# Kernel tuning notes

Hardware: AMD Instinct MI355X
Metric: run time of the kernel (lower is better)

## Reference

```python
import jax, jax.numpy as jnp
import numpy as np

AGENT_RADIUS = 0.5
SAFETY_DIST = 0.1
QP_ITERS = 300


def _qp_solve(p, G, h):
    """Batched QP: min_u 0.5 u^T u + p^T u  s.t.  G u <= h  (Q = I).
    Solved in the dual by projected gradient ascent (differentiable, fixed iters).
    p: [B,2], G: [B,m,2], h: [B,m] -> u: [B,2]
    """
    GGt = jnp.einsum('bmi,bni->bmn', G, G)                 # [B,m,m]
    q = jnp.einsum('bmi,bi->bm', G, p) + h                 # [B,m]
    # Lipschitz upper bound per sample (Frobenius norm of GG^T)
    L = jnp.sqrt(jnp.sum(GGt * GGt, axis=(1, 2))) + 1e-6   # [B]
    alpha = (1.0 / L)[:, None]

    def step(lam, _):
        grad = jnp.einsum('bmn,bn->bm', GGt, lam) + q
        lam = jnp.maximum(lam - alpha * grad, 0.0)
        return lam, None

    lam0 = jnp.zeros_like(h)
    lam, _ = jax.lax.scan(step, lam0, None, length=QP_ITERS)
    u = -p - jnp.einsum('bmi,bm->bi', G, lam)
    return u


def setup_inputs() -> dict:
    key = jax.random.key(0)
    ks = jax.random.split(key, 20)
    B, F, H1, H2 = 8192, 8, 1024, 512

    def w(k, i, o):
        return (jax.random.normal(k, (i, o), jnp.float32) / np.sqrt(i)).astype(jnp.float32)

    obs_xy = jax.random.uniform(ks[17], (8, 2), jnp.float32, -10.0, 10.0)
    obs_r = jax.random.uniform(ks[18], (8, 1), jnp.float32, 0.3, 0.8)
    return {
        'x': jax.random.normal(ks[0], (B, F), jnp.float32),
        'mean': 0.1 * jax.random.normal(ks[1], (F,), jnp.float32),
        'std': jax.random.uniform(ks[2], (F,), jnp.float32, 0.5, 1.5),
        'W1': w(ks[3], F, H1), 'b1': jnp.zeros((H1,), jnp.float32),
        'W21': w(ks[4], H1, H2), 'b21': jnp.zeros((H2,), jnp.float32),
        'W22': w(ks[5], H1, H2), 'b22': jnp.zeros((H2,), jnp.float32),
        'W23': w(ks[6], H1, H2), 'b23': jnp.zeros((H2,), jnp.float32),
        'W31': w(ks[7], H2, 2), 'b31': jnp.zeros((2,), jnp.float32),
        'W32': w(ks[8], H2, 2), 'b32': jnp.zeros((2,), jnp.float32),
        'W33': w(ks[9], H2, 1), 'b33': jnp.zeros((1,), jnp.float32),
        'obstacles': jnp.concatenate([obs_xy, obs_r], axis=1),  # [8,3] (x,y,r)
        'sgn': 1,
    }


def reference(x, mean, std, W1, b1, W21, b21, W22, b22, W23, b23,
              W31, b31, W32, b32, W33, b33, obstacles, sgn):
    B = x.shape[0]
    x0 = x * std + mean                                   # un-normalized state [B,8]

    h1 = jax.nn.relu(x @ W1 + b1)
    x21 = jax.nn.relu(h1 @ W21 + b21)
    x22 = jax.nn.relu(h1 @ W22 + b22)
    x23 = jax.nn.relu(h1 @ W23 + b23)
    x31 = x21 @ W31 + b31                                 # QP linear term p [B,2]
    x32 = 4.0 * jax.nn.sigmoid(x22 @ W32 + b32)           # CBF gains p1,p2 [B,2]
    x33 = 4.0 * jax.nn.sigmoid(x23 @ W33 + b33)           # liveness gain (unused, smg off)

    px, py, theta, v = x0[:, 0], x0[:, 1], x0[:, 2], x0[:, 3]
    st, ct = jnp.sin(theta)[:, None], jnp.cos(theta)[:, None]
    vb = v[:, None]

    # static obstacles broadcast to batch + opponent as last obstacle -> [B, m]
    ox = jnp.concatenate([jnp.broadcast_to(obstacles[:, 0][None], (B, obstacles.shape[0])), x0[:, 4:5]], axis=1)
    oy = jnp.concatenate([jnp.broadcast_to(obstacles[:, 1][None], (B, obstacles.shape[0])), x0[:, 5:6]], axis=1)
    orad = jnp.concatenate([jnp.broadcast_to(obstacles[:, 2][None], (B, obstacles.shape[0])),
                            jnp.full((B, 1), AGENT_RADIUS, x0.dtype)], axis=1)

    R = AGENT_RADIUS + orad + SAFETY_DIST
    dx = px[:, None] - ox                                  # [B,m]
    dy = py[:, None] - oy

    barrier = dx * dx + dy * dy - R * R
    barrier_dot = 2.0 * dx * vb * ct + 2.0 * dy * vb * st
    Lf2b = (2.0 * v * v)[:, None]
    LgLfbu1 = -2.0 * dx * vb * st + 2.0 * dy * vb * ct
    LgLfbu2 = 2.0 * dx * ct + 2.0 * dy * st
    G = jnp.stack([-LgLfbu1, -LgLfbu2], axis=-1)           # [B,m,2]
    p1, p2 = x32[:, 0:1], x32[:, 1:2]
    h = Lf2b + (p1 + p2) * barrier_dot + p1 * p2 * barrier # [B,m]

    u = _qp_solve(x31, G, h)                               # [B,2]
    return u
```

## Files before the change

kernel.cpp:

```cpp
#include <hip/hip_runtime.h>
#include <cstdint>
#include <cstddef>

typedef unsigned short u16;
typedef u16   u16x8  __attribute__((ext_vector_type(8)));
typedef u16   u16x4  __attribute__((ext_vector_type(4)));
typedef __bf16 bf16x8 __attribute__((ext_vector_type(8)));
typedef float f32x4  __attribute__((ext_vector_type(4)));
typedef float f32x2  __attribute__((ext_vector_type(2)));

__device__ __forceinline__ float bf2f(u16 v) {
  unsigned int u = ((unsigned int)v) << 16;
  return __builtin_bit_cast(float, u);
}
__device__ __forceinline__ u16 f2bf(float f) {
  unsigned int x = __builtin_bit_cast(unsigned int, f);
  x += 0x7fffu + ((x >> 16) & 1u);
  return (u16)(x >> 16);
}

__device__ __forceinline__ void gld_lds16(const u16* g, u16* l) {
  __builtin_amdgcn_global_load_lds(
      (const __attribute__((address_space(1))) unsigned int*)g,
      (__attribute__((address_space(3))) unsigned int*)l, 16, 0, 0);
}

__global__ __launch_bounds__(256) void k_tr(const float* __restrict__ W21,
                                            const float* __restrict__ W22,
                                            u16* __restrict__ Wt) {
  __shared__ u16 s[64][65];
  const int b   = blockIdx.x;
  const int mat = b >> 7;
  const int tt  = b & 127;
  const int k0  = (tt >> 3) * 64;
  const int n0  = (tt & 7) * 64;
  const float* W = mat ? W22 : W21;
  const int tx = threadIdx.x & 63;
  const int ty = threadIdx.x >> 6;
#pragma unroll
  for (int i = 0; i < 16; ++i) {
    int r = i * 4 + ty;
    s[r][tx] = f2bf(W[(size_t)(k0 + r) * 512 + n0 + tx]);
  }
  __syncthreads();
  const int nbase = mat * 512 + n0;
#pragma unroll
  for (int i = 0; i < 16; ++i) {
    int r = i * 4 + ty;
    Wt[(size_t)(nbase + r) * 1024 + k0 + tx] = s[tx][r];
  }
}

__global__ __launch_bounds__(256) void k_h1(const float* __restrict__ x,
                                            const float* __restrict__ W1,
                                            const float* __restrict__ b1,
                                            u16* __restrict__ h1) {
  const int row = blockIdx.x;
  const int c4  = threadIdx.x * 4;
  const float* xr = x + (size_t)row * 8;
  f32x4 acc = *(const f32x4*)(b1 + c4);
#pragma unroll
  for (int f = 0; f < 8; ++f) {
    float xv = xr[f];
    f32x4 wv = *(const f32x4*)(W1 + f * 1024 + c4);
#pragma unroll
    for (int e = 0; e < 4; ++e) acc[e] = fmaf(xv, wv[e], acc[e]);
  }
  u16x4 o;
#pragma unroll
  for (int e = 0; e < 4; ++e) o[e] = f2bf(fmaxf(acc[e], 0.f));
  *(u16x4*)(h1 + (size_t)row * 1024 + c4) = o;
}

__global__ __launch_bounds__(256) void k_gemm(const u16* __restrict__ A,
                                              const u16* __restrict__ Bt,
                                              const float* __restrict__ b21,
                                              const float* __restrict__ b22,
                                              u16* __restrict__ X2) {
  constexpr int K = 1024;
  constexpr int BK = 32;
  __shared__ u16 As[128 * BK];
  __shared__ u16 Bs[128 * BK];

  const int t    = threadIdx.x;
  const int row0 = blockIdx.y * 128;
  const int col0 = blockIdx.x * 128;
  const int w    = t >> 6;
  const int lane = t & 63;
  const int wr   = w >> 1, wc = w & 1;
  const int lrow = lane & 15;
  const int lk   = (lane >> 4) * 8;

  const int cA0 = t, cA1 = 256 + t;
  const int cB0 = t, cB1 = 256 + t;
  const u16* gA0 = A  + (size_t)(row0 + (cA0 >> 2)) * K + (cA0 & 3) * 8;
  const u16* gA1 = A  + (size_t)(row0 + (cA1 >> 2)) * K + (cA1 & 3) * 8;
  const u16* gB0 = Bt + (size_t)(col0 + (cB0 >> 2)) * K + (cB0 & 3) * 8;
  const u16* gB1 = Bt + (size_t)(col0 + (cB1 >> 2)) * K + (cB1 & 3) * 8;
  u16* lA0 = As + cA0 * 8;
  u16* lA1 = As + cA1 * 8;
  u16* lB0 = Bs + cB0 * 8;
  u16* lB1 = Bs + cB1 * 8;

  f32x4 acc[4][4];
#pragma unroll
  for (int i = 0; i < 4; ++i)
#pragma unroll
    for (int j = 0; j < 4; ++j) acc[i][j] = f32x4{0.f, 0.f, 0.f, 0.f};

  for (int kt = 0; kt < K / BK; ++kt) {
    gld_lds16(gA0, lA0);
    gld_lds16(gA1, lA1);
    gld_lds16(gB0, lB0);
    gld_lds16(gB1, lB1);
    gA0 += BK; gA1 += BK; gB0 += BK; gB1 += BK;
    __syncthreads();

    bf16x8 af[4], bfr[4];
#pragma unroll
    for (int i = 0; i < 4; ++i)
      af[i] = __builtin_bit_cast(bf16x8,
          *(const u16x8*)(As + (wr * 64 + i * 16 + lrow) * BK + lk));
#pragma unroll
    for (int j = 0; j < 4; ++j)
      bfr[j] = __builtin_bit_cast(bf16x8,
          *(const u16x8*)(Bs + (wc * 64 + j * 16 + lrow) * BK + lk));
#pragma unroll
    for (int i = 0; i < 4; ++i)
#pragma unroll
      for (int j = 0; j < 4; ++j)
        acc[i][j] = __builtin_amdgcn_mfma_f32_16x16x32_bf16(af[i], bfr[j], acc[i][j], 0, 0, 0);
    __syncthreads();
  }

#pragma unroll
  for (int j = 0; j < 4; ++j) {
    int col = col0 + wc * 64 + j * 16 + lrow;
    float bias = (col < 512) ? b21[col] : b22[col - 512];
#pragma unroll
    for (int i = 0; i < 4; ++i) {
      int rbase = row0 + wr * 64 + i * 16 + (lane >> 4) * 4;
#pragma unroll
      for (int rr = 0; rr < 4; ++rr) {
        float v = acc[i][j][rr] + bias;
        X2[(size_t)(rbase + rr) * 1024 + col] = f2bf(fmaxf(v, 0.f));
      }
    }
  }
}

__global__ __launch_bounds__(256) void k_head(const u16* __restrict__ X2,
                                              const float* __restrict__ W31,
                                              const float* __restrict__ W32,
                                              float* __restrict__ head) {
  const int wv   = threadIdx.x >> 6;
  const int lane = threadIdx.x & 63;
  const int r    = blockIdx.x * 4 + wv;
  const u16* row = X2 + (size_t)r * 1024;

  u16x8 v0 = *(const u16x8*)(row + lane * 8);
  u16x8 v1 = *(const u16x8*)(row + 512 + lane * 8);
  const f32x4* w31p = (const f32x4*)(W31 + lane * 16);
  const f32x4* w32p = (const f32x4*)(W32 + lane * 16);

  float a0x = 0.f, a0y = 0.f, a1x = 0.f, a1y = 0.f;
#pragma unroll
  for (int i = 0; i < 4; ++i) {
    f32x4 wa = w31p[i];
    float e0 = bf2f(v0[2 * i]), e1 = bf2f(v0[2 * i + 1]);
    a0x = fmaf(e0, wa[0], a0x); a0y = fmaf(e0, wa[1], a0y);
    a0x = fmaf(e1, wa[2], a0x); a0y = fmaf(e1, wa[3], a0y);
    f32x4 wb = w32p[i];
    float f0 = bf2f(v1[2 * i]), f1 = bf2f(v1[2 * i + 1]);
    a1x = fmaf(f0, wb[0], a1x); a1y = fmaf(f0, wb[1], a1y);
    a1x = fmaf(f1, wb[2], a1x); a1y = fmaf(f1, wb[3], a1y);
  }
#pragma unroll
  for (int m = 32; m >= 1; m >>= 1) {
    a0x += __shfl_xor(a0x, m, 64);
    a0y += __shfl_xor(a0y, m, 64);
    a1x += __shfl_xor(a1x, m, 64);
    a1y += __shfl_xor(a1y, m, 64);
  }
  if (lane == 0)
    *(f32x4*)(head + 4 * (size_t)r) = f32x4{a0x, a0y, a1x, a1y};
}

__global__ __launch_bounds__(64) void k_qp(const float* __restrict__ x,
                                           const float* __restrict__ mean_,
                                           const float* __restrict__ std_,
                                           const float* __restrict__ head,
                                           const float* __restrict__ b31,
                                           const float* __restrict__ b32,
                                           const float* __restrict__ obstacles,
                                           float* __restrict__ out) {
  const int r = blockIdx.x * 64 + threadIdx.x;
  f32x4 hd = *(const f32x4*)(head + 4 * (size_t)r);
  float p0  = hd[0] + b31[0];
  float p1v = hd[1] + b31[1];
  float pp1 = 4.f / (1.f + expf(-(hd[2] + b32[0])));
  float pp2 = 4.f / (1.f + expf(-(hd[3] + b32[1])));

  const f32x4* xp = (const f32x4*)(x + (size_t)r * 8);
  f32x4 xa = xp[0], xb = xp[1];
  float px = xa[0] * std_[0] + mean_[0];
  float py = xa[1] * std_[1] + mean_[1];
  float th = xa[2] * std_[2] + mean_[2];
  float v  = xa[3] * std_[3] + mean_[3];
  float ax = xb[0] * std_[4] + mean_[4];
  float ay = xb[1] * std_[5] + mean_[5];
  float st = sinf(th), ct = cosf(th);
  float Lf2b = 2.f * v * v;

  float G0[9], G1[9], q[9];
  float s00 = 0.f, s01 = 0.f, s11 = 0.f;
#pragma unroll
  for (int m = 0; m < 9; ++m) {
    float ox, oy, orad;
    if (m < 8) {
      ox = obstacles[m * 3]; oy = obstacles[m * 3 + 1]; orad = obstacles[m * 3 + 2];
    } else { ox = ax; oy = ay; orad = 0.5f; }
    float R  = 0.6f + orad;
    float dx = px - ox, dy = py - oy;
    float bar  = dx * dx + dy * dy - R * R;
    float dct  = dx * ct + dy * st;
    float bdot = 2.f * v * dct;
    float g0 = 2.f * v * (dx * st - dy * ct);
    float g1 = -2.f * dct;
    float h  = Lf2b + (pp1 + pp2) * bdot + pp1 * pp2 * bar;
    G0[m] = g0; G1[m] = g1;
    q[m] = g0 * p0 + g1 * p1v + h;
    s00 += g0 * g0; s01 += g0 * g1; s11 += g1 * g1;
  }
  float L = sqrtf(s00 * s00 + 2.f * s01 * s01 + s11 * s11) + 1e-6f;
  float alpha = 1.f / L;

  float lam[9];
#pragma unroll
  for (int m = 0; m < 9; ++m) lam[m] = 0.f;
  for (int it = 0; it < 300; ++it) {
    float pr0[9], pr1[9];
#pragma unroll
    for (int m = 0; m < 9; ++m) { pr0[m] = G0[m] * lam[m]; pr1[m] = G1[m] * lam[m]; }
    float t0 = (((pr0[0] + pr0[1]) + (pr0[2] + pr0[3])) +
                ((pr0[4] + pr0[5]) + (pr0[6] + pr0[7]))) + pr0[8];
    float t1 = (((pr1[0] + pr1[1]) + (pr1[2] + pr1[3])) +
                ((pr1[4] + pr1[5]) + (pr1[6] + pr1[7]))) + pr1[8];
#pragma unroll
    for (int m = 0; m < 9; ++m) {
      float g = fmaf(G0[m], t0, fmaf(G1[m], t1, q[m]));
      lam[m] = fmaxf(fmaf(-alpha, g, lam[m]), 0.f);
    }
  }
  float u0 = -p0, u1 = -p1v;
#pragma unroll
  for (int m = 0; m < 9; ++m) { u0 = fmaf(-G0[m], lam[m], u0); u1 = fmaf(-G1[m], lam[m], u1); }
  *(f32x2*)(out + 2 * (size_t)r) = f32x2{u0, u1};
}

extern "C" void kernel_launch(void* const* d_in, const int* in_sizes, int n_in,
                              void* d_out, int out_size, void* d_ws, size_t ws_size,
                              hipStream_t stream) {
  const float* x    = (const float*)d_in[0];
  const float* mean_= (const float*)d_in[1];
  const float* std_ = (const float*)d_in[2];
  const float* W1   = (const float*)d_in[3];
  const float* b1   = (const float*)d_in[4];
  const float* W21  = (const float*)d_in[5];
  const float* b21  = (const float*)d_in[6];
  const float* W22  = (const float*)d_in[7];
  const float* b22  = (const float*)d_in[8];
  const float* W31  = (const float*)d_in[11];
  const float* b31  = (const float*)d_in[12];
  const float* W32  = (const float*)d_in[13];
  const float* b32  = (const float*)d_in[14];
  const float* obst = (const float*)d_in[17];
  float* out = (float*)d_out;

  char* ws = (char*)d_ws;
  u16*   Wt   = (u16*)ws;
  u16*   h1   = (u16*)(ws + (size_t)(1 << 21));
  u16*   X2   = (u16*)(ws + (size_t)(1 << 21) + (size_t)(1 << 24));
  float* head = (float*)(ws + (size_t)(1 << 21) + 2 * (size_t)(1 << 24));

  k_tr  <<<256, 256, 0, stream>>>(W21, W22, Wt);
  k_h1  <<<8192, 256, 0, stream>>>(x, W1, b1, h1);
  k_gemm<<<dim3(8, 64), 256, 0, stream>>>(h1, Wt, b21, b22, X2);
  k_head<<<2048, 256, 0, stream>>>(X2, W31, W32, head);
  k_qp  <<<128, 64, 0, stream>>>(x, mean_, std_, head, b31, b32, obst, out);
}
```

Measured before the change: 172.5 us.

## Double-buffer GEMM LDS tiles with register-staged prefetch two tiles ahead

Replaces the direct global-to-LDS loads in the bf16 MFMA GEMM with ordinary vector loads into registers, staged two K-tiles ahead, and a double-buffered LDS. This removes one barrier per iteration and lets global memory latency overlap with the MFMA work on the current tile. In exchange it uses more registers and twice the LDS, which may lower occupancy, and every element now takes an extra register-to-LDS store.

```diff
diff --git a/kernel.cpp b/kernel.cpp
--- a/kernel.cpp
+++ b/kernel.cpp
@@ -17,12 +17,6 @@
   unsigned int x = __builtin_bit_cast(unsigned int, f);
   x += 0x7fffu + ((x >> 16) & 1u);
   return (u16)(x >> 16);
-}
-
-__device__ __forceinline__ void gld_lds16(const u16* g, u16* l) {
-  __builtin_amdgcn_global_load_lds(
-      (const __attribute__((address_space(1))) unsigned int*)g,
-      (__attribute__((address_space(3))) unsigned int*)l, 16, 0, 0);
 }
 
 __global__ __launch_bounds__(256) void k_tr(const float* __restrict__ W21,
@@ -77,10 +71,11 @@
                                               const float* __restrict__ b21,
                                               const float* __restrict__ b22,
                                               u16* __restrict__ X2) {
-  constexpr int K = 1024;
+  constexpr int K  = 1024;
   constexpr int BK = 32;
-  __shared__ u16 As[128 * BK];
-  __shared__ u16 Bs[128 * BK];
+  constexpr int NT = K / BK;
+  __shared__ u16 As[2][128 * BK];
+  __shared__ u16 Bs[2][128 * BK];
 
   const int t    = threadIdx.x;
   const int row0 = blockIdx.y * 128;
@@ -91,16 +86,12 @@
   const int lrow = lane & 15;
   const int lk   = (lane >> 4) * 8;
 
-  const int cA0 = t, cA1 = 256 + t;
-  const int cB0 = t, cB1 = 256 + t;
-  const u16* gA0 = A  + (size_t)(row0 + (cA0 >> 2)) * K + (cA0 & 3) * 8;
-  const u16* gA1 = A  + (size_t)(row0 + (cA1 >> 2)) * K + (cA1 & 3) * 8;
-  const u16* gB0 = Bt + (size_t)(col0 + (cB0 >> 2)) * K + (cB0 & 3) * 8;
-  const u16* gB1 = Bt + (size_t)(col0 + (cB1 >> 2)) * K + (cB1 & 3) * 8;
-  u16* lA0 = As + cA0 * 8;
-  u16* lA1 = As + cA1 * 8;
-  u16* lB0 = Bs + cB0 * 8;
-  u16* lB1 = Bs + cB1 * 8;
+  const int c0 = t, c1 = 256 + t;
+  const u16* gA0 = A  + (size_t)(row0 + (c0 >> 2)) * K + (c0 & 3) * 8;
+  const u16* gA1 = A  + (size_t)(row0 + (c1 >> 2)) * K + (c1 & 3) * 8;
+  const u16* gB0 = Bt + (size_t)(col0 + (c0 >> 2)) * K + (c0 & 3) * 8;
+  const u16* gB1 = Bt + (size_t)(col0 + (c1 >> 2)) * K + (c1 & 3) * 8;
+  const int lo0 = c0 * 8, lo1 = c1 * 8;
 
   f32x4 acc[4][4];
 #pragma unroll
@@ -108,29 +99,53 @@
 #pragma unroll
     for (int j = 0; j < 4; ++j) acc[i][j] = f32x4{0.f, 0.f, 0.f, 0.f};
 
-  for (int kt = 0; kt < K / BK; ++kt) {
-    gld_lds16(gA0, lA0);
-    gld_lds16(gA1, lA1);
-    gld_lds16(gB0, lB0);
-    gld_lds16(gB1, lB1);
-    gA0 += BK; gA1 += BK; gB0 += BK; gB1 += BK;
+  {
+    u16x8 ta0 = *(const u16x8*)gA0;
+    u16x8 ta1 = *(const u16x8*)gA1;
+    u16x8 tb0 = *(const u16x8*)gB0;
+    u16x8 tb1 = *(const u16x8*)gB1;
+    *(u16x8*)(As[0] + lo0) = ta0;
+    *(u16x8*)(As[0] + lo1) = ta1;
+    *(u16x8*)(Bs[0] + lo0) = tb0;
+    *(u16x8*)(Bs[0] + lo1) = tb1;
+  }
+  u16x8 na0 = *(const u16x8*)(gA0 + BK);
+  u16x8 na1 = *(const u16x8*)(gA1 + BK);
+  u16x8 nb0 = *(const u16x8*)(gB0 + BK);
+  u16x8 nb1 = *(const u16x8*)(gB1 + BK);
+
+  for (int kt = 0; kt < NT; ++kt) {
+    const int cur = kt & 1, nxt = cur ^ 1;
     __syncthreads();
+
+    const int koff = (kt + 2 < NT ? kt + 2 : NT - 1) * BK;
+    u16x8 fa0 = *(const u16x8*)(gA0 + koff);
+    u16x8 fa1 = *(const u16x8*)(gA1 + koff);
+    u16x8 fb0 = *(const u16x8*)(gB0 + koff);
+    u16x8 fb1 = *(const u16x8*)(gB1 + koff);
 
     bf16x8 af[4], bfr[4];
 #pragma unroll
     for (int i = 0; i < 4; ++i)
       af[i] = __builtin_bit_cast(bf16x8,
-          *(const u16x8*)(As + (wr * 64 + i * 16 + lrow) * BK + lk));
+          *(const u16x8*)(As[cur] + (wr * 64 + i * 16 + lrow) * BK + lk));
 #pragma unroll
     for (int j = 0; j < 4; ++j)
       bfr[j] = __builtin_bit_cast(bf16x8,
-          *(const u16x8*)(Bs + (wc * 64 + j * 16 + lrow) * BK + lk));
+          *(const u16x8*)(Bs[cur] + (wc * 64 + j * 16 + lrow) * BK + lk));
 #pragma unroll
     for (int i = 0; i < 4; ++i)
 #pragma unroll
       for (int j = 0; j < 4; ++j)
         acc[i][j] = __builtin_amdgcn_mfma_f32_16x16x32_bf16(af[i], bfr[j], acc[i][j], 0, 0, 0);
-    __syncthreads();
+
+    if (kt + 1 < NT) {
+      *(u16x8*)(As[nxt] + lo0) = na0;
+      *(u16x8*)(As[nxt] + lo1) = na1;
+      *(u16x8*)(Bs[nxt] + lo0) = nb0;
+      *(u16x8*)(Bs[nxt] + lo1) = nb1;
+    }
+    na0 = fa0; na1 = fa1; nb0 = fb0; nb1 = fb1;
   }
 
 #pragma unroll
```

After: 171.0 us. About the same (-0.8%).
